# Performance work log

Measured on AMD Instinct MI355X. Metric: run time of the kernel, lower is better.

Reference implementation:

```python
import jax, jax.numpy as jnp
import numpy as np

NEG = -1e9
CLIP = 10.0  # tanh clipping constant for SingleHeadAttention logits


def layer_norm(x, g, b, eps=1e-5):
    mu = jnp.mean(x, axis=-1, keepdims=True)
    var = jnp.var(x, axis=-1, keepdims=True)
    return (x - mu) * jax.lax.rsqrt(var + eps) * g + b


def setup_inputs() -> dict:
    key = jax.random.key(0)
    ks = jax.random.split(key, 16)
    B, A, N, E, Hf = 4096, 16, 128, 128, 128
    s = 0.02
    inp = {
        "agent_embed": jax.random.normal(ks[0], (B, A, E), jnp.float32),
        "city_embed": jax.random.normal(ks[1], (B, N, E), jnp.float32),
        "acts": jax.random.randint(ks[2], (B, A), 0, N, jnp.int32),
        # cross-attention layer params
        "Wq": jax.random.normal(ks[3], (E, E), jnp.float32) * s,
        "Wk": jax.random.normal(ks[4], (E, E), jnp.float32) * s,
        "Wv": jax.random.normal(ks[5], (E, E), jnp.float32) * s,
        "Wo": jax.random.normal(ks[6], (E, E), jnp.float32) * s,
        "ln1_g": jnp.ones((E,), jnp.float32),
        "ln1_b": jnp.zeros((E,), jnp.float32),
        "W1": jax.random.normal(ks[7], (E, Hf), jnp.float32) * s,
        "b1": jnp.zeros((Hf,), jnp.float32),
        "W2": jax.random.normal(ks[8], (Hf, E), jnp.float32) * s,
        "b2": jnp.zeros((E,), jnp.float32),
        "ln2_g": jnp.ones((E,), jnp.float32),
        "ln2_b": jnp.zeros((E,), jnp.float32),
        # single-head attention params
        "Wq_s": jax.random.normal(ks[9], (E, E), jnp.float32) * s,
        "Wk_s": jax.random.normal(ks[10], (E, E), jnp.float32) * s,
    }
    return inp


def reference(agent_embed, city_embed, acts, Wq, Wk, Wv, Wo, ln1_g, ln1_b,
              W1, b1, W2, b2, ln2_g, ln2_b, Wq_s, Wk_s):
    B, A, E = agent_embed.shape
    H = 8
    dh = E // H

    # ---- conflict mask construction ----
    eq = acts[:, :, None] == acts[:, None, :]            # [B,A,A] True = same city
    ident = jnp.eye(A, dtype=bool)[None]                 # [1,A,A]
    conflict = jnp.where(acts[:, :, None] == 0, ident, eq)
    mask = ~conflict                                     # True = blocked in attention

    # ---- gather per-agent selected city embeddings ----
    selected = jnp.take_along_axis(city_embed, acts[:, :, None].astype(jnp.int32), axis=1)  # [B,A,E]

    # ---- cross-attention layer (num_layers = 1) ----
    cac = selected
    q = (cac @ Wq).reshape(B, A, H, dh)
    k = (agent_embed @ Wk).reshape(B, A, H, dh)
    v = (agent_embed @ Wv).reshape(B, A, H, dh)
    scores = jnp.einsum("bqhd,bkhd->bhqk", q, k) / np.sqrt(dh).astype(np.float32)
    scores = jnp.where(mask[:, None, :, :], NEG, scores)
    attn = jax.nn.softmax(scores, axis=-1)
    out = jnp.einsum("bhqk,bkhd->bqhd", attn, v).reshape(B, A, E) @ Wo
    h = layer_norm(cac + out, ln1_g, ln1_b)
    ffn = jax.nn.relu(h @ W1 + b1) @ W2 + b2
    cac = layer_norm(h + ffn, ln2_g, ln2_b)

    # ---- single-head attention producing logits [B,A,A] ----
    qs = cac @ Wq_s
    ks_ = agent_embed @ Wk_s
    logits = jnp.einsum("bqe,bke->bqk", qs, ks_) / np.sqrt(E).astype(np.float32)
    logits = CLIP * jnp.tanh(logits)
    logits = jnp.where(mask, NEG, logits)
    return logits
```

## Files before the change

### kernel.cpp

```cpp
#include <hip/hip_runtime.h>
#include <hip/hip_bf16.h>
#include <math.h>

typedef __attribute__((ext_vector_type(8))) short bfrag;
typedef __attribute__((ext_vector_type(4))) float f32x4;

#define LDK 136

__global__ __launch_bounds__(256) void prep_weights(
    const float* __restrict__ Wq, const float* __restrict__ Wk,
    const float* __restrict__ Wv, const float* __restrict__ Wo,
    const float* __restrict__ W1, const float* __restrict__ W2,
    const float* __restrict__ Wqs, const float* __restrict__ Wks,
    __hip_bfloat16* __restrict__ out)
{
    const float* Ws[8] = {Wq, Wk, Wv, Wo, W1, W2, Wqs, Wks};
    const float* W = Ws[blockIdx.x];
    __hip_bfloat16* o = out + (size_t)blockIdx.x * 16384;
    for (int idx = threadIdx.x; idx < 16384; idx += 256) {
        int n = idx >> 7, k = idx & 127;
        o[idx] = __float2bfloat16(W[k * 128 + n]);
    }
}

__device__ __forceinline__ void mm_acc(const __hip_bfloat16* A,
                                       const __hip_bfloat16* __restrict__ wT,
                                       int m, int quad, int ct0, f32x4 acc[2][2])
{
    const f32x4 z = {0.f, 0.f, 0.f, 0.f};
    acc[0][0] = z; acc[0][1] = z; acc[1][0] = z; acc[1][1] = z;
#pragma unroll
    for (int kk = 0; kk < 128; kk += 32) {
        const int k = kk + quad * 8;
        bfrag a0 = *(const bfrag*)(A + m * LDK + k);
        bfrag a1 = *(const bfrag*)(A + (16 + m) * LDK + k);
        bfrag b0 = *(const bfrag*)(wT + (size_t)(ct0 * 16 + m) * 128 + k);
        bfrag b1 = *(const bfrag*)(wT + (size_t)((ct0 + 1) * 16 + m) * 128 + k);
        acc[0][0] = __builtin_amdgcn_mfma_f32_16x16x32_bf16(a0, b0, acc[0][0], 0, 0, 0);
        acc[1][0] = __builtin_amdgcn_mfma_f32_16x16x32_bf16(a1, b0, acc[1][0], 0, 0, 0);
        acc[0][1] = __builtin_amdgcn_mfma_f32_16x16x32_bf16(a0, b1, acc[0][1], 0, 0, 0);
        acc[1][1] = __builtin_amdgcn_mfma_f32_16x16x32_bf16(a1, b1, acc[1][1], 0, 0, 0);
    }
}

__device__ __forceinline__ void ln_step(const __hip_bfloat16* in, __hip_bfloat16* outb,
                                        const float* __restrict__ g,
                                        const float* __restrict__ bb, int tid)
{
    int row = tid >> 3;
    int part = tid & 7;
    const __hip_bfloat16* p = in + row * LDK + part * 16;
    float x[16];
#pragma unroll
    for (int j = 0; j < 16; ++j) x[j] = __bfloat162float(p[j]);
    float s = 0.f, s2 = 0.f;
#pragma unroll
    for (int j = 0; j < 16; ++j) { s += x[j]; s2 += x[j] * x[j]; }
#pragma unroll
    for (int off = 1; off < 8; off <<= 1) {
        s += __shfl_xor(s, off, 64);
        s2 += __shfl_xor(s2, off, 64);
    }
    float mu = s * (1.f / 128.f);
    float var = s2 * (1.f / 128.f) - mu * mu;
    float sc = rsqrtf(var + 1e-5f);
    __hip_bfloat16* o = outb + row * LDK + part * 16;
#pragma unroll
    for (int j = 0; j < 16; ++j) {
        int c = part * 16 + j;
        o[j] = __float2bfloat16((x[j] - mu) * sc * g[c] + bb[c]);
    }
}

__global__ __launch_bounds__(256) void fused_model(
    const float* __restrict__ agent_embed,
    const float* __restrict__ city_embed,
    const int* __restrict__ acts,
    const __hip_bfloat16* __restrict__ wts,
    const float* __restrict__ ln1g, const float* __restrict__ ln1b,
    const float* __restrict__ b1, const float* __restrict__ b2,
    const float* __restrict__ ln2g, const float* __restrict__ ln2b,
    float* __restrict__ out)
{
    __shared__ __hip_bfloat16 sXA[32 * LDK];
    __shared__ __hip_bfloat16 sXS[32 * LDK];
    __shared__ __hip_bfloat16 sK [32 * LDK];
    __shared__ __hip_bfloat16 sV [32 * LDK];
    __shared__ __hip_bfloat16 sKS[32 * LDK];
    __shared__ __hip_bfloat16 sQ [32 * LDK];
    __shared__ int sActs[32];

    const int tid = threadIdx.x;
    const int lane = tid & 63;
    const int wave = tid >> 6;
    const int m = lane & 15;
    const int quad = lane >> 4;
    const int ct0 = wave * 2;
    const int b0 = blockIdx.x * 2;

    if (tid < 32) sActs[tid] = acts[b0 * 16 + tid];
    {
        const float4* src = (const float4*)(agent_embed + (size_t)b0 * 16 * 128);
#pragma unroll
        for (int p = 0; p < 4; ++p) {
            int v = p * 256 + tid;
            float4 f = src[v];
            int flat = v * 4;
            __hip_bfloat16* d = sXA + (flat >> 7) * LDK + (flat & 127);
            d[0] = __float2bfloat16(f.x); d[1] = __float2bfloat16(f.y);
            d[2] = __float2bfloat16(f.z); d[3] = __float2bfloat16(f.w);
        }
    }
    {
        int r = tid >> 3, part = tid & 7;
        int b = b0 + (r >> 4), i = r & 15;
        int act = acts[b * 16 + i];
        const float4* src = (const float4*)(city_embed + ((size_t)b * 128 + act) * 128);
        __hip_bfloat16* d = sXS + r * LDK + part * 16;
#pragma unroll
        for (int p = 0; p < 4; ++p) {
            float4 f = src[part * 4 + p];
            d[p * 4 + 0] = __float2bfloat16(f.x); d[p * 4 + 1] = __float2bfloat16(f.y);
            d[p * 4 + 2] = __float2bfloat16(f.z); d[p * 4 + 3] = __float2bfloat16(f.w);
        }
    }
    __syncthreads();

    f32x4 acc[2][2];
#define STORE_PLAIN(dst)                                                        \
    for (int rt = 0; rt < 2; ++rt)                                              \
        for (int c = 0; c < 2; ++c)                                             \
            for (int r = 0; r < 4; ++r)                                         \
                dst[(rt * 16 + quad * 4 + r) * LDK + (ct0 + c) * 16 + m] =      \
                    __float2bfloat16(acc[rt][c][r]);

    mm_acc(sXA, wts + 1 * 16384, m, quad, ct0, acc); STORE_PLAIN(sK);
    mm_acc(sXA, wts + 2 * 16384, m, quad, ct0, acc); STORE_PLAIN(sV);
    mm_acc(sXA, wts + 7 * 16384, m, quad, ct0, acc); STORE_PLAIN(sKS);
    mm_acc(sXS, wts + 0 * 16384, m, quad, ct0, acc); STORE_PLAIN(sQ);
    __syncthreads();

    {
        int g = tid >> 7;
        int h = (tid >> 4) & 7;
        int q = tid & 15;
        int row = g * 16 + q;
        int aq = sActs[row];
        float Qr[16];
        const __hip_bfloat16* qp = sQ + row * LDK + h * 16;
#pragma unroll
        for (int d = 0; d < 16; ++d) Qr[d] = __bfloat162float(qp[d]);
        float s[16];
        float mx = -1e30f;
#pragma unroll
        for (int k = 0; k < 16; ++k) {
            const __hip_bfloat16* kp = sK + (g * 16 + k) * LDK + h * 16;
            float dot = 0.f;
#pragma unroll
            for (int d = 0; d < 16; ++d) dot += Qr[d] * __bfloat162float(kp[d]);
            dot *= 0.25f;
            int ak = sActs[g * 16 + k];
            bool conflict = (aq == 0) ? (q == k) : (aq == ak);
            if (!conflict) dot = -1e9f;
            s[k] = dot;
            mx = fmaxf(mx, dot);
        }
        float sum = 0.f;
#pragma unroll
        for (int k = 0; k < 16; ++k) { s[k] = __expf(s[k] - mx); sum += s[k]; }
        float inv = 1.f / sum;
        float o[16];
#pragma unroll
        for (int d = 0; d < 16; ++d) o[d] = 0.f;
#pragma unroll
        for (int k = 0; k < 16; ++k) {
            const __hip_bfloat16* vp = sV + (g * 16 + k) * LDK + h * 16;
            float p = s[k];
#pragma unroll
            for (int d = 0; d < 16; ++d) o[d] += p * __bfloat162float(vp[d]);
        }
        __hip_bfloat16* op = sXA + row * LDK + h * 16;
#pragma unroll
        for (int d = 0; d < 16; ++d) op[d] = __float2bfloat16(o[d] * inv);
    }
    __syncthreads();

    mm_acc(sXA, wts + 3 * 16384, m, quad, ct0, acc);
    for (int rt = 0; rt < 2; ++rt)
        for (int c = 0; c < 2; ++c)
            for (int r = 0; r < 4; ++r) {
                int row = rt * 16 + quad * 4 + r, col = (ct0 + c) * 16 + m;
                float v = acc[rt][c][r] + __bfloat162float(sXS[row * LDK + col]);
                sQ[row * LDK + col] = __float2bfloat16(v);
            }
    __syncthreads();

    ln_step(sQ, sK, ln1g, ln1b, tid);
    __syncthreads();

    mm_acc(sK, wts + 4 * 16384, m, quad, ct0, acc);
    for (int rt = 0; rt < 2; ++rt)
        for (int c = 0; c < 2; ++c) {
            int col = (ct0 + c) * 16 + m;
            float bias = b1[col];
            for (int r = 0; r < 4; ++r) {
                int row = rt * 16 + quad * 4 + r;
                float v = fmaxf(acc[rt][c][r] + bias, 0.f);
                sV[row * LDK + col] = __float2bfloat16(v);
            }
        }
    __syncthreads();

    mm_acc(sV, wts + 5 * 16384, m, quad, ct0, acc);
    for (int rt = 0; rt < 2; ++rt)
        for (int c = 0; c < 2; ++c) {
            int col = (ct0 + c) * 16 + m;
            float bias = b2[col];
            for (int r = 0; r < 4; ++r) {
                int row = rt * 16 + quad * 4 + r;
                float v = acc[rt][c][r] + bias + __bfloat162float(sK[row * LDK + col]);
                sXA[row * LDK + col] = __float2bfloat16(v);
            }
        }
    __syncthreads();

    ln_step(sXA, sXS, ln2g, ln2b, tid);
    __syncthreads();

    mm_acc(sXS, wts + 6 * 16384, m, quad, ct0, acc);
    STORE_PLAIN(sK);
    __syncthreads();

    if (wave < 2) {
        int g = wave;
        f32x4 la = {0.f, 0.f, 0.f, 0.f};
#pragma unroll
        for (int kk = 0; kk < 128; kk += 32) {
            int k = kk + quad * 8;
            bfrag a = *(const bfrag*)(sK + (g * 16 + m) * LDK + k);
            bfrag b = *(const bfrag*)(sKS + (g * 16 + m) * LDK + k);
            la = __builtin_amdgcn_mfma_f32_16x16x32_bf16(a, b, la, 0, 0, 0);
        }
        int b = b0 + g;
        int kcol = m;
        int ak = sActs[g * 16 + kcol];
#pragma unroll
        for (int r = 0; r < 4; ++r) {
            int q = quad * 4 + r;
            int aq = sActs[g * 16 + q];
            float v = la[r] * 0.0883883476483184f;
            v = 10.f * tanhf(v);
            bool conflict = (aq == 0) ? (q == kcol) : (aq == ak);
            out[((size_t)b * 16 + q) * 16 + kcol] = conflict ? v : -1e9f;
        }
    }
#undef STORE_PLAIN
}

extern "C" void kernel_launch(void* const* d_in, const int* in_sizes, int n_in,
                              void* d_out, int out_size, void* d_ws, size_t ws_size,
                              hipStream_t stream)
{
    const float* agent = (const float*)d_in[0];
    const float* city  = (const float*)d_in[1];
    const int*   acts  = (const int*)d_in[2];
    const float* Wq  = (const float*)d_in[3];
    const float* Wk  = (const float*)d_in[4];
    const float* Wv  = (const float*)d_in[5];
    const float* Wo  = (const float*)d_in[6];
    const float* l1g = (const float*)d_in[7];
    const float* l1b = (const float*)d_in[8];
    const float* W1  = (const float*)d_in[9];
    const float* b1  = (const float*)d_in[10];
    const float* W2  = (const float*)d_in[11];
    const float* b2  = (const float*)d_in[12];
    const float* l2g = (const float*)d_in[13];
    const float* l2b = (const float*)d_in[14];
    const float* Wqs = (const float*)d_in[15];
    const float* Wks = (const float*)d_in[16];
    float* out = (float*)d_out;

    int B = in_sizes[2] / 16;
    __hip_bfloat16* wts = (__hip_bfloat16*)d_ws;

    prep_weights<<<8, 256, 0, stream>>>(Wq, Wk, Wv, Wo, W1, W2, Wqs, Wks, wts);
    fused_model<<<B / 2, 256, 0, stream>>>(agent, city, acts, wts, l1g, l1b,
                                           b1, b2, l2g, l2b, out);
}
```

Measured before the change: 435.3 us.

## Compute cross-attention heads with MFMA and transpose weights through shared memory

Replaces the per-thread scalar attention (dot products, softmax, weighted V sum) with two 16x16x32 bf16 MFMA calls per (batch,head) pair. The K dimension is zero-padded from a shared zero buffer, and the softmax normalisation is done with cross-lane shuffles. V is stored in a per-head tiled layout so the MFMA B fragments can be loaded directly. The weight-prep kernel now transposes through shared memory with coalesced float4 loads and vector stores. The softmax drops max-subtraction, which risks overflow for large scores, and uses bf16 probabilities. Several store loops also gain unroll pragmas.

```diff
diff --git a/kernel.cpp b/kernel.cpp
--- a/kernel.cpp
+++ b/kernel.cpp
@@ -4,6 +4,7 @@
 
 typedef __attribute__((ext_vector_type(8))) short bfrag;
 typedef __attribute__((ext_vector_type(4))) float f32x4;
+typedef __attribute__((ext_vector_type(4))) short short4v;
 
 #define LDK 136
 
@@ -14,12 +15,28 @@
     const float* __restrict__ Wqs, const float* __restrict__ Wks,
     __hip_bfloat16* __restrict__ out)
 {
+    __shared__ __align__(16) __hip_bfloat16 t[128 * 129];
     const float* Ws[8] = {Wq, Wk, Wv, Wo, W1, W2, Wqs, Wks};
     const float* W = Ws[blockIdx.x];
     __hip_bfloat16* o = out + (size_t)blockIdx.x * 16384;
-    for (int idx = threadIdx.x; idx < 16384; idx += 256) {
-        int n = idx >> 7, k = idx & 127;
-        o[idx] = __float2bfloat16(W[k * 128 + n]);
+#pragma unroll
+    for (int p = 0; p < 16; ++p) {
+        int v = p * 256 + threadIdx.x;
+        float4 f = ((const float4*)W)[v];
+        int flat = v * 4;
+        __hip_bfloat16* d = t + (flat >> 7) * 129 + (flat & 127);
+        d[0] = __float2bfloat16(f.x); d[1] = __float2bfloat16(f.y);
+        d[2] = __float2bfloat16(f.z); d[3] = __float2bfloat16(f.w);
+    }
+    __syncthreads();
+#pragma unroll
+    for (int p = 0; p < 8; ++p) {
+        int i = p * 256 + threadIdx.x;
+        int n = i >> 4, k0 = (i & 15) * 8;
+        __hip_bfloat16 v[8];
+#pragma unroll
+        for (int j = 0; j < 8; ++j) v[j] = t[(k0 + j) * 129 + n];
+        *(bfrag*)(o + n * 128 + k0) = *(const bfrag*)v;
     }
 }
 
@@ -82,12 +99,13 @@
     const float* __restrict__ ln2g, const float* __restrict__ ln2b,
     float* __restrict__ out)
 {
-    __shared__ __hip_bfloat16 sXA[32 * LDK];
-    __shared__ __hip_bfloat16 sXS[32 * LDK];
-    __shared__ __hip_bfloat16 sK [32 * LDK];
-    __shared__ __hip_bfloat16 sV [32 * LDK];
-    __shared__ __hip_bfloat16 sKS[32 * LDK];
-    __shared__ __hip_bfloat16 sQ [32 * LDK];
+    __shared__ __align__(16) __hip_bfloat16 sXA[32 * LDK];
+    __shared__ __align__(16) __hip_bfloat16 sXS[32 * LDK];
+    __shared__ __align__(16) __hip_bfloat16 sK [32 * LDK];
+    __shared__ __align__(16) __hip_bfloat16 sV [32 * LDK];
+    __shared__ __align__(16) __hip_bfloat16 sKS[32 * LDK];
+    __shared__ __align__(16) __hip_bfloat16 sQ [32 * LDK];
+    __shared__ __align__(16) __hip_bfloat16 sZero[8];
     __shared__ int sActs[32];
 
     const int tid = threadIdx.x;
@@ -99,6 +117,7 @@
     const int b0 = blockIdx.x * 2;
 
     if (tid < 32) sActs[tid] = acts[b0 * 16 + tid];
+    if (tid < 8) sZero[tid] = __float2bfloat16(0.f);
     {
         const float4* src = (const float4*)(agent_embed + (size_t)b0 * 16 * 128);
 #pragma unroll
@@ -135,59 +154,67 @@
                     __float2bfloat16(acc[rt][c][r]);
 
     mm_acc(sXA, wts + 1 * 16384, m, quad, ct0, acc); STORE_PLAIN(sK);
-    mm_acc(sXA, wts + 2 * 16384, m, quad, ct0, acc); STORE_PLAIN(sV);
+    mm_acc(sXA, wts + 2 * 16384, m, quad, ct0, acc);
+#pragma unroll
+    for (int rt = 0; rt < 2; ++rt)
+#pragma unroll
+        for (int c = 0; c < 2; ++c) {
+            __hip_bfloat16 pk[4];
+#pragma unroll
+            for (int r = 0; r < 4; ++r) pk[r] = __float2bfloat16(acc[rt][c][r]);
+            *(short4v*)(sV + ((rt * 8 + ct0 + c) * 16 + m) * 16 + quad * 4) =
+                *(const short4v*)pk;
+        }
     mm_acc(sXA, wts + 7 * 16384, m, quad, ct0, acc); STORE_PLAIN(sKS);
     mm_acc(sXS, wts + 0 * 16384, m, quad, ct0, acc); STORE_PLAIN(sQ);
     __syncthreads();
 
     {
-        int g = tid >> 7;
-        int h = (tid >> 4) & 7;
-        int q = tid & 15;
-        int row = g * 16 + q;
-        int aq = sActs[row];
-        float Qr[16];
-        const __hip_bfloat16* qp = sQ + row * LDK + h * 16;
-#pragma unroll
-        for (int d = 0; d < 16; ++d) Qr[d] = __bfloat162float(qp[d]);
-        float s[16];
-        float mx = -1e30f;
-#pragma unroll
-        for (int k = 0; k < 16; ++k) {
-            const __hip_bfloat16* kp = sK + (g * 16 + k) * LDK + h * 16;
-            float dot = 0.f;
-#pragma unroll
-            for (int d = 0; d < 16; ++d) dot += Qr[d] * __bfloat162float(kp[d]);
-            dot *= 0.25f;
-            int ak = sActs[g * 16 + k];
-            bool conflict = (aq == 0) ? (q == k) : (aq == ak);
-            if (!conflict) dot = -1e9f;
-            s[k] = dot;
-            mx = fmaxf(mx, dot);
-        }
-        float sum = 0.f;
-#pragma unroll
-        for (int k = 0; k < 16; ++k) { s[k] = __expf(s[k] - mx); sum += s[k]; }
-        float inv = 1.f / sum;
-        float o[16];
-#pragma unroll
-        for (int d = 0; d < 16; ++d) o[d] = 0.f;
-#pragma unroll
-        for (int k = 0; k < 16; ++k) {
-            const __hip_bfloat16* vp = sV + (g * 16 + k) * LDK + h * 16;
-            float p = s[k];
-#pragma unroll
-            for (int d = 0; d < 16; ++d) o[d] += p * __bfloat162float(vp[d]);
-        }
-        __hip_bfloat16* op = sXA + row * LDK + h * 16;
-#pragma unroll
-        for (int d = 0; d < 16; ++d) op[d] = __float2bfloat16(o[d] * inv);
+        const f32x4 z4 = {0.f, 0.f, 0.f, 0.f};
+#pragma unroll
+        for (int pp = 0; pp < 4; ++pp) {
+            const int p = wave * 4 + pp;
+            const int g = p >> 3, h = p & 7;
+            const __hip_bfloat16* qa = (quad < 2)
+                ? sQ + (g * 16 + m) * LDK + h * 16 + quad * 8 : sZero;
+            const __hip_bfloat16* kb = (quad < 2)
+                ? sK + (g * 16 + m) * LDK + h * 16 + quad * 8 : sZero;
+            f32x4 sc = __builtin_amdgcn_mfma_f32_16x16x32_bf16(
+                *(const bfrag*)qa, *(const bfrag*)kb, z4, 0, 0, 0);
+            const int ak = sActs[g * 16 + m];
+#pragma unroll
+            for (int r = 0; r < 4; ++r) {
+                int q = quad * 4 + r;
+                int aqv = sActs[g * 16 + q];
+                bool keep = (aqv == 0) ? (q == m) : (aqv == ak);
+                float e = keep ? __expf(sc[r] * 0.25f) : 0.f;
+                float s = e;
+                s += __shfl_xor(s, 1, 16);
+                s += __shfl_xor(s, 2, 16);
+                s += __shfl_xor(s, 4, 16);
+                s += __shfl_xor(s, 8, 16);
+                sQ[(g * 16 + q) * LDK + h * 16 + m] = __float2bfloat16(__fdividef(e, s));
+            }
+            const __hip_bfloat16* pa = (quad < 2)
+                ? sQ + (g * 16 + m) * LDK + h * 16 + quad * 8 : sZero;
+            const __hip_bfloat16* vb = (quad < 2)
+                ? sV + ((g * 8 + h) * 16 + m) * 16 + quad * 8 : sZero;
+            f32x4 o4 = __builtin_amdgcn_mfma_f32_16x16x32_bf16(
+                *(const bfrag*)pa, *(const bfrag*)vb, z4, 0, 0, 0);
+#pragma unroll
+            for (int r = 0; r < 4; ++r)
+                sXA[(g * 16 + quad * 4 + r) * LDK + h * 16 + m] =
+                    __float2bfloat16(o4[r]);
+        }
     }
     __syncthreads();
 
     mm_acc(sXA, wts + 3 * 16384, m, quad, ct0, acc);
+#pragma unroll
     for (int rt = 0; rt < 2; ++rt)
+#pragma unroll
         for (int c = 0; c < 2; ++c)
+#pragma unroll
             for (int r = 0; r < 4; ++r) {
                 int row = rt * 16 + quad * 4 + r, col = (ct0 + c) * 16 + m;
                 float v = acc[rt][c][r] + __bfloat162float(sXS[row * LDK + col]);
@@ -199,23 +226,28 @@
     __syncthreads();
 
     mm_acc(sK, wts + 4 * 16384, m, quad, ct0, acc);
+#pragma unroll
     for (int rt = 0; rt < 2; ++rt)
+#pragma unroll
         for (int c = 0; c < 2; ++c) {
             int col = (ct0 + c) * 16 + m;
             float bias = b1[col];
+#pragma unroll
             for (int r = 0; r < 4; ++r) {
                 int row = rt * 16 + quad * 4 + r;
-                float v = fmaxf(acc[rt][c][r] + bias, 0.f);
-                sV[row * LDK + col] = __float2bfloat16(v);
+                sV[row * LDK + col] = __float2bfloat16(fmaxf(acc[rt][c][r] + bias, 0.f));
             }
         }
     __syncthreads();
 
     mm_acc(sV, wts + 5 * 16384, m, quad, ct0, acc);
+#pragma unroll
     for (int rt = 0; rt < 2; ++rt)
+#pragma unroll
         for (int c = 0; c < 2; ++c) {
             int col = (ct0 + c) * 16 + m;
             float bias = b2[col];
+#pragma unroll
             for (int r = 0; r < 4; ++r) {
                 int row = rt * 16 + quad * 4 + r;
                 float v = acc[rt][c][r] + bias + __bfloat162float(sK[row * LDK + col]);
```

New measurement: 442.1 us. Within noise of the previous version (+1.6%).
